# Optimization experiments

Measured on AMD Instinct MI355X. Metric: run time of the kernel, lower is better.

Reference implementation:

```python
import jax, jax.numpy as jnp
import numpy as np

N_NODES = 100000
N_EDGES = 1_600_000
D_IN = 128
D_OUT = 128


def setup_inputs() -> dict:
    key = jax.random.key(0)
    k1, k2, k3 = jax.random.split(key, 3)
    input_matrix = jax.random.normal(k1, (N_NODES, D_IN), dtype=jnp.float32)
    adjacency_coo_matrix = jax.random.randint(k2, (2, N_EDGES), 0, N_NODES, dtype=jnp.int64)
    # xavier-uniform-style init for the weight matrix
    limit = float(np.sqrt(6.0 / (D_IN + D_OUT)))
    weights_matrix = jax.random.uniform(k3, (D_IN, D_OUT), dtype=jnp.float32, minval=-limit, maxval=limit)
    return {
        "input_matrix": input_matrix,
        "adjacency_coo_matrix": adjacency_coo_matrix,
        "weights_matrix": weights_matrix,
    }


def reference(input_matrix, adjacency_coo_matrix, weights_matrix):
    # Edge-wise gathers (the irregular-access pattern from the torch code)
    src_idx = adjacency_coo_matrix[0]
    dst_idx = adjacency_coo_matrix[1]
    neighbors = input_matrix[dst_idx]  # [E, D_IN] gather of neighbor features
    # Mean-aggregate neighbor features onto each src node
    agg = jax.ops.segment_sum(neighbors, src_idx, num_segments=N_NODES)  # [N, D_IN]
    deg = jax.ops.segment_sum(jnp.ones((neighbors.shape[0],), dtype=input_matrix.dtype),
                              src_idx, num_segments=N_NODES)  # [N]
    mean_agg = agg / jnp.maximum(deg, 1.0)[:, None]
    # Linear transform with the layer weight matrix
    out = mean_agg @ weights_matrix  # [N, D_OUT]
    return out
```

## Files before the change

### kernel.cpp

```cpp
#include <hip/hip_runtime.h>

#define NN 100000
#define NE 1600000
#define DD 128
#define CAP 64
#define SLICES 8
#define SLICE_N 12500
#define FILL_BLOCKS 2048
#define GEMM_BLOCKS ((NN + 63) / 64)

typedef __bf16 bf16x8 __attribute__((ext_vector_type(8)));
typedef float  f32x4  __attribute__((ext_vector_type(4)));

__device__ __forceinline__ unsigned int f2bf(float f) {
    unsigned int u = __float_as_uint(f);
    return (u + 0x7FFFu + ((u >> 16) & 1u)) >> 16;
}
__device__ __forceinline__ float bflo(unsigned int u) { return __uint_as_float(u << 16); }
__device__ __forceinline__ float bfhi(unsigned int u) { return __uint_as_float(u & 0xFFFF0000u); }

__global__ __launch_bounds__(256) void k_cvtw(const float* __restrict__ W,
                                              unsigned short* __restrict__ wtb)
{
    const int idx = blockIdx.x * 256 + threadIdx.x;
    if (idx >= DD * DD) return;
    const int k = idx >> 7, n = idx & 127;
    wtb[n * DD + k] = (unsigned short)f2bf(W[idx]);
}

__global__ __launch_bounds__(256) void k_fused(const int* __restrict__ adj,
                                               int* __restrict__ cnt,
                                               int* __restrict__ edge_dst,
                                               const float* __restrict__ x,
                                               const unsigned short* __restrict__ wtb,
                                               unsigned short* __restrict__ y)
{
    if (blockIdx.x < FILL_BLOCKS) {
        const int slice = blockIdx.x & 7;
        const int w     = blockIdx.x >> 3;
        const int lo    = slice * SLICE_N;
        const uint4* src4 = (const uint4*)adj;
        const uint4* dst4 = (const uint4*)(adj + NE);
        const int ngroups = NE / 4;

        for (int g = w * 256 + (int)threadIdx.x; g < ngroups; g += (FILL_BLOCKS / 8) * 256) {
            const uint4 s4 = src4[g];
            const uint4 d4 = dst4[g];
            #pragma unroll
            for (int j = 0; j < 4; ++j) {
                const int s = (j == 0) ? s4.x : (j == 1) ? s4.y : (j == 2) ? s4.z : s4.w;
                const int d = (j == 0) ? d4.x : (j == 1) ? d4.y : (j == 2) ? d4.z : d4.w;
                if ((unsigned)(s - lo) < (unsigned)SLICE_N) {
                    int slot = atomicAdd(&cnt[s], 1);
                    if (slot < CAP) edge_dst[(size_t)s * CAP + slot] = d;
                }
            }
        }
        return;
    }

    const int bid = blockIdx.x - FILL_BLOCKS;
    const int wave = threadIdx.x >> 6;
    const int lane = threadIdx.x & 63;
    const int quad = lane >> 4;
    const int l16  = lane & 15;
    const int mbase = bid * 64 + wave * 16;
    const int m = mbase + l16;

    bf16x8 a[4];
    if (m < NN) {
        const float* arow = x + (size_t)m * DD + quad * 8;
        #pragma unroll
        for (int ks = 0; ks < 4; ++ks) {
            const float4 f0 = *(const float4*)(arow + ks * 32);
            const float4 f1 = *(const float4*)(arow + ks * 32 + 4);
            uint4 p;
            p.x = f2bf(f0.x) | (f2bf(f0.y) << 16);
            p.y = f2bf(f0.z) | (f2bf(f0.w) << 16);
            p.z = f2bf(f1.x) | (f2bf(f1.y) << 16);
            p.w = f2bf(f1.z) | (f2bf(f1.w) << 16);
            a[ks] = __builtin_bit_cast(bf16x8, p);
        }
    } else {
        const uint4 z = make_uint4(0, 0, 0, 0);
        #pragma unroll
        for (int ks = 0; ks < 4; ++ks) a[ks] = __builtin_bit_cast(bf16x8, z);
    }

    #pragma unroll
    for (int nt = 0; nt < 8; ++nt) {
        f32x4 c = {0.f, 0.f, 0.f, 0.f};
        const unsigned short* bcol = wtb + (nt * 16 + l16) * DD + quad * 8;
        #pragma unroll
        for (int ks = 0; ks < 4; ++ks) {
            const bf16x8 b = __builtin_bit_cast(bf16x8, *(const uint4*)(bcol + ks * 32));
            c = __builtin_amdgcn_mfma_f32_16x16x32_bf16(a[ks], b, c, 0, 0, 0);
        }
        #pragma unroll
        for (int r = 0; r < 4; ++r) {
            const int row = mbase + quad * 4 + r;
            if (row < NN)
                y[(size_t)row * DD + nt * 16 + l16] = (unsigned short)f2bf(c[r]);
        }
    }
}

__global__ __launch_bounds__(256) void k_agg2(const unsigned short* __restrict__ y,
                                              const int* __restrict__ cnt,
                                              const int* __restrict__ edge_dst,
                                              float* __restrict__ out)
{
    const int n    = blockIdx.x * 4 + (threadIdx.x >> 6);
    const int lane = threadIdx.x & 63;
    const int eg   = lane >> 4;
    const int h    = lane & 15;
    int deg = cnt[n];
    if (deg > CAP) deg = CAP;
    const int* el = edge_dst + (size_t)n * CAP;

    float acc[8] = {0.f,0.f,0.f,0.f,0.f,0.f,0.f,0.f};

    int i = eg;
    for (; i + 4 < deg; i += 8) {
        const int d0 = el[i];
        const int d1 = el[i + 4];
        const uint4 p0 = *(const uint4*)(y + (size_t)d0 * DD + h * 8);
        const uint4 p1 = *(const uint4*)(y + (size_t)d1 * DD + h * 8);
        acc[0] += bflo(p0.x); acc[1] += bfhi(p0.x);
        acc[2] += bflo(p0.y); acc[3] += bfhi(p0.y);
        acc[4] += bflo(p0.z); acc[5] += bfhi(p0.z);
        acc[6] += bflo(p0.w); acc[7] += bfhi(p0.w);
        acc[0] += bflo(p1.x); acc[1] += bfhi(p1.x);
        acc[2] += bflo(p1.y); acc[3] += bfhi(p1.y);
        acc[4] += bflo(p1.z); acc[5] += bfhi(p1.z);
        acc[6] += bflo(p1.w); acc[7] += bfhi(p1.w);
    }
    for (; i < deg; i += 4) {
        const int d0 = el[i];
        const uint4 p0 = *(const uint4*)(y + (size_t)d0 * DD + h * 8);
        acc[0] += bflo(p0.x); acc[1] += bfhi(p0.x);
        acc[2] += bflo(p0.y); acc[3] += bfhi(p0.y);
        acc[4] += bflo(p0.z); acc[5] += bfhi(p0.z);
        acc[6] += bflo(p0.w); acc[7] += bfhi(p0.w);
    }

    #pragma unroll
    for (int j = 0; j < 8; ++j) {
        acc[j] += __shfl_xor(acc[j], 16, 64);
        acc[j] += __shfl_xor(acc[j], 32, 64);
    }

    if (eg == 0) {
        const float inv = 1.0f / fmaxf((float)deg, 1.0f);
        float* o = out + (size_t)n * DD + h * 8;
        float4 w0 = {acc[0]*inv, acc[1]*inv, acc[2]*inv, acc[3]*inv};
        float4 w1 = {acc[4]*inv, acc[5]*inv, acc[6]*inv, acc[7]*inv};
        *(float4*)(o + 0) = w0;
        *(float4*)(o + 4) = w1;
    }
}

extern "C" void kernel_launch(void* const* d_in, const int* in_sizes, int n_in,
                              void* d_out, int out_size, void* d_ws, size_t ws_size,
                              hipStream_t stream) {
    const float* x   = (const float*)d_in[0];
    const int*   adj = (const int*)d_in[1];
    const float* W   = (const float*)d_in[2];
    float* out = (float*)d_out;

    unsigned short* y   = (unsigned short*)d_ws;
    unsigned short* wtb = y + (size_t)NN * DD;
    int* cnt      = (int*)(wtb + DD * DD);
    int* edge_dst = cnt + NN;

    hipMemsetAsync(cnt, 0, NN * sizeof(int), stream);
    k_cvtw <<<DD * DD / 256, 256, 0, stream>>>(W, wtb);
    k_fused<<<FILL_BLOCKS + GEMM_BLOCKS, 256, 0, stream>>>(adj, cnt, edge_dst, x, wtb, y);
    k_agg2 <<<NN / 4, 256, 0, stream>>>(y, cnt, edge_dst, out);
}
```

Before: 256.2 us.

## Fold counter memset into weight prep, unroll fill and gather loops, widen GEMM tiles

Replaces the hipMemsetAsync with zeroing inside the weight-conversion kernel, which removes one launch. Halves the number of fill blocks and unrolls the fill loop two-deep so more loads are in flight. Each GEMM block now covers 128 rows in two 16-row subtiles per wave, with launch bounds set to 8 blocks per SM. The aggregation loop is unrolled to four gathers per iteration to raise memory-level parallelism. Fewer fill blocks could reduce atomic parallelism, and larger GEMM blocks reduce the block count.

```diff
diff --git a/kernel.cpp b/kernel.cpp
--- a/kernel.cpp
+++ b/kernel.cpp
@@ -4,10 +4,11 @@
 #define NE 1600000
 #define DD 128
 #define CAP 64
-#define SLICES 8
 #define SLICE_N 12500
-#define FILL_BLOCKS 2048
-#define GEMM_BLOCKS ((NN + 63) / 64)
+#define FILL_BLOCKS 1024
+#define BPS (FILL_BLOCKS / 8)
+#define GEMM_ROWS 128
+#define GEMM_BLOCKS ((NN + GEMM_ROWS - 1) / GEMM_ROWS)
 
 typedef __bf16 bf16x8 __attribute__((ext_vector_type(8)));
 typedef float  f32x4  __attribute__((ext_vector_type(4)));
@@ -19,21 +20,23 @@
 __device__ __forceinline__ float bflo(unsigned int u) { return __uint_as_float(u << 16); }
 __device__ __forceinline__ float bfhi(unsigned int u) { return __uint_as_float(u & 0xFFFF0000u); }
 
-__global__ __launch_bounds__(256) void k_cvtw(const float* __restrict__ W,
-                                              unsigned short* __restrict__ wtb)
+__global__ __launch_bounds__(256) void k_prep(const float* __restrict__ W,
+                                              unsigned short* __restrict__ wtb,
+                                              int* __restrict__ cnt)
 {
-    const int idx = blockIdx.x * 256 + threadIdx.x;
-    if (idx >= DD * DD) return;
+    const int idx = blockIdx.x * 256 + (int)threadIdx.x;
     const int k = idx >> 7, n = idx & 127;
     wtb[n * DD + k] = (unsigned short)f2bf(W[idx]);
-}
-
-__global__ __launch_bounds__(256) void k_fused(const int* __restrict__ adj,
-                                               int* __restrict__ cnt,
-                                               int* __restrict__ edge_dst,
-                                               const float* __restrict__ x,
-                                               const unsigned short* __restrict__ wtb,
-                                               unsigned short* __restrict__ y)
+    int4* c4 = (int4*)cnt;
+    for (int i = idx; i < NN / 4; i += DD * DD) c4[i] = make_int4(0, 0, 0, 0);
+}
+
+__global__ __launch_bounds__(256, 8) void k_fused(const int* __restrict__ adj,
+                                                  int* __restrict__ cnt,
+                                                  int* __restrict__ edge_dst,
+                                                  const float* __restrict__ x,
+                                                  const unsigned short* __restrict__ wtb,
+                                                  unsigned short* __restrict__ y)
 {
     if (blockIdx.x < FILL_BLOCKS) {
         const int slice = blockIdx.x & 7;
@@ -42,65 +45,83 @@
         const uint4* src4 = (const uint4*)adj;
         const uint4* dst4 = (const uint4*)(adj + NE);
         const int ngroups = NE / 4;
-
-        for (int g = w * 256 + (int)threadIdx.x; g < ngroups; g += (FILL_BLOCKS / 8) * 256) {
-            const uint4 s4 = src4[g];
-            const uint4 d4 = dst4[g];
-            #pragma unroll
-            for (int j = 0; j < 4; ++j) {
-                const int s = (j == 0) ? s4.x : (j == 1) ? s4.y : (j == 2) ? s4.z : s4.w;
-                const int d = (j == 0) ? d4.x : (j == 1) ? d4.y : (j == 2) ? d4.z : d4.w;
-                if ((unsigned)(s - lo) < (unsigned)SLICE_N) {
-                    int slot = atomicAdd(&cnt[s], 1);
-                    if (slot < CAP) edge_dst[(size_t)s * CAP + slot] = d;
-                }
-            }
-        }
+        const int stride  = BPS * 256;
+
+        #define PROC(s4, d4) do {                                                     \
+            _Pragma("unroll")                                                         \
+            for (int j = 0; j < 4; ++j) {                                             \
+                const int s = (j==0)?(int)(s4).x:(j==1)?(int)(s4).y:                  \
+                              (j==2)?(int)(s4).z:(int)(s4).w;                         \
+                const int d = (j==0)?(int)(d4).x:(j==1)?(int)(d4).y:                  \
+                              (j==2)?(int)(d4).z:(int)(d4).w;                         \
+                if ((unsigned)(s - lo) < (unsigned)SLICE_N) {                         \
+                    int slot = atomicAdd(&cnt[s], 1);                                 \
+                    if (slot < CAP) edge_dst[(size_t)s * CAP + slot] = d;             \
+                }                                                                     \
+            }                                                                         \
+        } while (0)
+
+        int g = w * 256 + (int)threadIdx.x;
+        for (; g + stride < ngroups; g += 2 * stride) {
+            const uint4 sa = src4[g],          da = dst4[g];
+            const uint4 sb = src4[g + stride], db = dst4[g + stride];
+            PROC(sa, da);
+            PROC(sb, db);
+        }
+        for (; g < ngroups; g += stride) {
+            const uint4 s4 = src4[g], d4 = dst4[g];
+            PROC(s4, d4);
+        }
+        #undef PROC
         return;
     }
 
-    const int bid = blockIdx.x - FILL_BLOCKS;
-    const int wave = threadIdx.x >> 6;
-    const int lane = threadIdx.x & 63;
+    const int bid  = blockIdx.x - FILL_BLOCKS;
+    const int wave = (int)threadIdx.x >> 6;
+    const int lane = (int)threadIdx.x & 63;
     const int quad = lane >> 4;
     const int l16  = lane & 15;
-    const int mbase = bid * 64 + wave * 16;
-    const int m = mbase + l16;
-
-    bf16x8 a[4];
-    if (m < NN) {
-        const float* arow = x + (size_t)m * DD + quad * 8;
+
+    #pragma unroll 1
+    for (int mt = 0; mt < 2; ++mt) {
+        const int mbase = bid * GEMM_ROWS + wave * 32 + mt * 16;
+        const int m = mbase + l16;
+
+        bf16x8 a[4];
+        if (m < NN) {
+            const float* arow = x + (size_t)m * DD + quad * 8;
+            #pragma unroll
+            for (int ks = 0; ks < 4; ++ks) {
+                const float4 f0 = *(const float4*)(arow + ks * 32);
+                const float4 f1 = *(const float4*)(arow + ks * 32 + 4);
+                uint4 p;
+                p.x = f2bf(f0.x) | (f2bf(f0.y) << 16);
+                p.y = f2bf(f0.z) | (f2bf(f0.w) << 16);
+                p.z = f2bf(f1.x) | (f2bf(f1.y) << 16);
+                p.w = f2bf(f1.z) | (f2bf(f1.w) << 16);
+                a[ks] = __builtin_bit_cast(bf16x8, p);
+            }
+        } else {
+            const uint4 z = make_uint4(0, 0, 0, 0);
+            #pragma unroll
+            for (int ks = 0; ks < 4; ++ks) a[ks] = __builtin_bit_cast(bf16x8, z);
+        }
+
         #pragma unroll
-        for (int ks = 0; ks < 4; ++ks) {
-            const float4 f0 = *(const float4*)(arow + ks * 32);
-            const float4 f1 = *(const float4*)(arow + ks * 32 + 4);
-            uint4 p;
-            p.x = f2bf(f0.x) | (f2bf(f0.y) << 16);
-            p.y = f2bf(f0.z) | (f2bf(f0.w) << 16);
-            p.z = f2bf(f1.x) | (f2bf(f1.y) << 16);
-            p.w = f2bf(f1.z) | (f2bf(f1.w) << 16);
-            a[ks] = __builtin_bit_cast(bf16x8, p);
-        }
-    } else {
-        const uint4 z = make_uint4(0, 0, 0, 0);
-        #pragma unroll
-        for (int ks = 0; ks < 4; ++ks) a[ks] = __builtin_bit_cast(bf16x8, z);
-    }
-
-    #pragma unroll
-    for (int nt = 0; nt < 8; ++nt) {
-        f32x4 c = {0.f, 0.f, 0.f, 0.f};
-        const unsigned short* bcol = wtb + (nt * 16 + l16) * DD + quad * 8;
-        #pragma unroll
-        for (int ks = 0; ks < 4; ++ks) {
-            const bf16x8 b = __builtin_bit_cast(bf16x8, *(const uint4*)(bcol + ks * 32));
-            c = __builtin_amdgcn_mfma_f32_16x16x32_bf16(a[ks], b, c, 0, 0, 0);
-        }
-        #pragma unroll
-        for (int r = 0; r < 4; ++r) {
-            const int row = mbase + quad * 4 + r;
-            if (row < NN)
-                y[(size_t)row * DD + nt * 16 + l16] = (unsigned short)f2bf(c[r]);
+        for (int nt = 0; nt < 8; ++nt) {
+            f32x4 c = {0.f, 0.f, 0.f, 0.f};
+            const unsigned short* bcol = wtb + (nt * 16 + l16) * DD + quad * 8;
+            #pragma unroll
+            for (int ks = 0; ks < 4; ++ks) {
+                const bf16x8 b = __builtin_bit_cast(bf16x8, *(const uint4*)(bcol + ks * 32));
+                c = __builtin_amdgcn_mfma_f32_16x16x32_bf16(a[ks], b, c, 0, 0, 0);
+            }
+            #pragma unroll
+            for (int r = 0; r < 4; ++r) {
+                const int row = mbase + quad * 4 + r;
+                if (row < NN)
+                    y[(size_t)row * DD + nt * 16 + l16] = (unsigned short)f2bf(c[r]);
+            }
         }
     }
 }
@@ -110,8 +131,8 @@
                                               const int* __restrict__ edge_dst,
                                               float* __restrict__ out)
 {
-    const int n    = blockIdx.x * 4 + (threadIdx.x >> 6);
-    const int lane = threadIdx.x & 63;
+    const int n    = blockIdx.x * 4 + ((int)threadIdx.x >> 6);
+    const int lane = (int)threadIdx.x & 63;
     const int eg   = lane >> 4;
     const int h    = lane & 15;
     int deg = cnt[n];
@@ -120,29 +141,38 @@
 
     float acc[8] = {0.f,0.f,0.f,0.f,0.f,0.f,0.f,0.f};
 
+    #define ACC(p) do {                                         \
+        acc[0] += bflo((p).x); acc[1] += bfhi((p).x);           \
+        acc[2] += bflo((p).y); acc[3] += bfhi((p).y);           \
+        acc[4] += bflo((p).z); acc[5] += bfhi((p).z);           \
+        acc[6] += bflo((p).w); acc[7] += bfhi((p).w);           \
+    } while (0)
+
     int i = eg;
+    for (; i + 12 < deg; i += 16) {
+        const int d0 = el[i];
+        const int d1 = el[i + 4];
+        const int d2 = el[i + 8];
+        const int d3 = el[i + 12];
+        const uint4 p0 = *(const uint4*)(y + (size_t)d0 * DD + h * 8);
+        const uint4 p1 = *(const uint4*)(y + (size_t)d1 * DD + h * 8);
+        const uint4 p2 = *(const uint4*)(y + (size_t)d2 * DD + h * 8);
+        const uint4 p3 = *(const uint4*)(y + (size_t)d3 * DD + h * 8);
+        ACC(p0); ACC(p1); ACC(p2); ACC(p3);
+    }
     for (; i + 4 < deg; i += 8) {
         const int d0 = el[i];
         const int d1 = el[i + 4];
         const uint4 p0 = *(const uint4*)(y + (size_t)d0 * DD + h * 8);
         const uint4 p1 = *(const uint4*)(y + (size_t)d1 * DD + h * 8);
-        acc[0] += bflo(p0.x); acc[1] += bfhi(p0.x);
-        acc[2] += bflo(p0.y); acc[3] += bfhi(p0.y);
-        acc[4] += bflo(p0.z); acc[5] += bfhi(p0.z);
-        acc[6] += bflo(p0.w); acc[7] += bfhi(p0.w);
-        acc[0] += bflo(p1.x); acc[1] += bfhi(p1.x);
-        acc[2] += bflo(p1.y); acc[3] += bfhi(p1.y);
-        acc[4] += bflo(p1.z); acc[5] += bfhi(p1.z);
-        acc[6] += bflo(p1.w); acc[7] += bfhi(p1.w);
+        ACC(p0); ACC(p1);
     }
     for (; i < deg; i += 4) {
         const int d0 = el[i];
         const uint4 p0 = *(const uint4*)(y + (size_t)d0 * DD + h * 8);
-        acc[0] += bflo(p0.x); acc[1] += bfhi(p0.x);
-        acc[2] += bflo(p0.y); acc[3] += bfhi(p0.y);
-        acc[4] += bflo(p0.z); acc[5] += bfhi(p0.z);
-        acc[6] += bflo(p0.w); acc[7] += bfhi(p0.w);
-    }
+        ACC(p0);
+    }
+    #undef ACC
 
     #pragma unroll
     for (int j = 0; j < 8; ++j) {
@@ -173,8 +203,7 @@
     int* cnt      = (int*)(wtb + DD * DD);
     int* edge_dst = cnt + NN;
 
-    hipMemsetAsync(cnt, 0, NN * sizeof(int), stream);
-    k_cvtw <<<DD * DD / 256, 256, 0, stream>>>(W, wtb);
+    k_prep <<<DD * DD / 256, 256, 0, stream>>>(W, wtb, cnt);
     k_fused<<<FILL_BLOCKS + GEMM_BLOCKS, 256, 0, stream>>>(adj, cnt, edge_dst, x, wtb, y);
     k_agg2 <<<NN / 4, 256, 0, stream>>>(y, cnt, edge_dst, out);
 }
```

Measured after the change: 303.7 us. 1.19x slower.
